# Kernel tuning notes

Hardware: AMD Instinct MI355X
Metric: run time of the kernel (lower is better)

Reference implementation:

```python
import jax, jax.numpy as jnp
import numpy as np

N_ATOMS = 200_000
N_EDGES = 10_000_000
N_MOL = 128


def setup_inputs() -> dict:
    key = jax.random.key(0)
    k1, k2, k3, k4, k5, k6, k7 = jax.random.split(key, 7)
    dEdRij = jax.random.normal(k1, (N_EDGES, 3), dtype=jnp.float32)
    Rij = jax.random.normal(k2, (N_EDGES, 3), dtype=jnp.float32)
    R = jax.random.normal(k3, (N_ATOMS, 3), dtype=jnp.float32)
    # Non-degenerate cells: ~10 Angstrom cubic boxes with small perturbation
    cell = jnp.eye(3, dtype=jnp.float32) * 10.0 + 0.1 * jax.random.normal(k4, (N_MOL, 3, 3), dtype=jnp.float32)
    idx_i = jax.random.randint(k5, (N_EDGES,), 0, N_ATOMS, dtype=jnp.int32)
    idx_j = jax.random.randint(k6, (N_EDGES,), 0, N_ATOMS, dtype=jnp.int32)
    idx_m = jnp.sort(jax.random.randint(k7, (N_ATOMS,), 0, N_MOL, dtype=jnp.int32))
    return {"dEdRij": dEdRij, "Rij": Rij, "R": R, "cell": cell,
            "idx_i": idx_i, "idx_j": idx_j, "idx_m": idx_m}


def reference(dEdRij, Rij, R, cell, idx_i, idx_j, idx_m):
    N = R.shape[0]
    M = cell.shape[0]
    # Forces: F = sum_{edges into i} dE/dRij - sum_{edges from j} dE/dRij
    forces = jnp.zeros_like(R).at[idx_i].add(dEdRij).at[idx_j].add(-dEdRij)
    # Per-edge outer product [E,3,3]: Rij[:, :, None] * dEdRij[:, None, :]
    stress_edge = dEdRij[:, None, :] * Rij[:, :, None]
    # Scatter to atoms, then reduce atoms -> molecules
    stress_i = jnp.zeros((N, 3, 3), dtype=R.dtype).at[idx_i].add(stress_edge)
    stress = jax.ops.segment_sum(stress_i, idx_m, num_segments=M)  # [M,3,3]
    # Cell volume via scalar triple product a . (b x c)
    volume = jnp.sum(cell[:, 0, :] * jnp.cross(cell[:, 1, :], cell[:, 2, :]), axis=1)  # [M]
    stress_out = (stress / volume[:, None, None]).reshape(M * 3, 3)
    return forces, stress_out
```

## Files before the change

### kernel.cpp

```cpp
#include <hip/hip_runtime.h>
#include <hip/hip_bf16.h>
#include <hip/hip_fp16.h>

#define N_MOL 128
#define STRESS_FLOATS (N_MOL * 9)
#define NB 128
#define APB 1563
#define NPAD (NB * APB)
#define EPB 1024
#define K_PT 4
#define BLK 256
#define RS_SLICES 64

__global__ void zero_f32_kernel(float* __restrict__ p, size_t n) {
    size_t i = (size_t)blockIdx.x * blockDim.x + threadIdx.x;
    if (i < n) p[i] = 0.f;
}

__device__ __forceinline__ unsigned short h16(float v) {
    return __half_as_ushort(__float2half_rn(v));
}

__global__ void __launch_bounds__(256)
scatter_kernel(const float* __restrict__ dEdRij,
               const float* __restrict__ Rij,
               const int*   __restrict__ idx_i,
               const int*   __restrict__ idx_j,
               const int*   __restrict__ idx_m,
               uint2* __restrict__ rec,
               int*   __restrict__ cnt,
               float* __restrict__ spart,
               int e0_chunk, int n_edges_chunk, int CAP)
{
    __shared__ int           hist[NB];
    __shared__ int           excl[NB];
    __shared__ int           cur[NB];
    __shared__ int           shiftb[NB];
    __shared__ float         smem[STRESS_FLOATS];
    __shared__ uint2         stg[EPB * 2];
    __shared__ unsigned char stgb[EPB * 2];

    for (int t = threadIdx.x; t < NB; t += blockDim.x) hist[t] = 0;
    for (int t = threadIdx.x; t < STRESS_FLOATS; t += blockDim.x) smem[t] = 0.f;
    __syncthreads();

    const int be0 = e0_chunk + blockIdx.x * EPB;
    const int be1 = min(be0 + EPB, e0_chunk + n_edges_chunk);

    int ei[K_PT], ej[K_PT];
    #pragma unroll
    for (int k = 0; k < K_PT; ++k) {
        const int e = be0 + k * BLK + threadIdx.x;
        ei[k] = -1; ej[k] = -1;
        if (e < be1) {
            ei[k] = idx_i[e];
            ej[k] = idx_j[e];
            atomicAdd(&hist[ei[k] / APB], 1);
            atomicAdd(&hist[ej[k] / APB], 1);
        }
    }
    __syncthreads();

    if (threadIdx.x < 64) {
        const int l = threadIdx.x;
        const int a = hist[2 * l], b = hist[2 * l + 1];
        int s = a + b;
        #pragma unroll
        for (int off = 1; off < 64; off <<= 1) {
            const int v = __shfl_up(s, off, 64);
            if (l >= off) s += v;
        }
        const int excl_pair = s - (a + b);
        excl[2 * l]     = excl_pair;
        excl[2 * l + 1] = excl_pair + a;
    }
    __syncthreads();

    for (int t = threadIdx.x; t < NB; t += blockDim.x) {
        const int h  = hist[t];
        const int ex = excl[t];
        const int g  = h ? atomicAdd(&cnt[t], h) : 0;
        cur[t]    = ex;
        shiftb[t] = t * CAP + g - ex;
    }
    __syncthreads();

    #pragma unroll
    for (int k = 0; k < K_PT; ++k) {
        const int e = be0 + k * BLK + threadIdx.x;
        if (e >= be1) continue;
        const int i = ei[k], j = ej[k];
        const float dx = dEdRij[3*e+0], dy = dEdRij[3*e+1], dz = dEdRij[3*e+2];
        const float rx = Rij[3*e+0],    ry = Rij[3*e+1],    rz = Rij[3*e+2];

        const int m = idx_m[i];
        float* s = &smem[m * 9];
        atomicAdd(&s[0], rx * dx);
        atomicAdd(&s[1], rx * dy);
        atomicAdd(&s[2], rx * dz);
        atomicAdd(&s[3], ry * dx);
        atomicAdd(&s[4], ry * dy);
        atomicAdd(&s[5], ry * dz);
        atomicAdd(&s[6], rz * dx);
        atomicAdd(&s[7], rz * dy);
        atomicAdd(&s[8], rz * dz);

        const int bi = i / APB;
        const int li = i - bi * APB;
        uint2 q;
        q.x = ((unsigned)li << 16) | h16(dx);
        q.y = (unsigned)h16(dy) | ((unsigned)h16(dz) << 16);
        int p = atomicAdd(&cur[bi], 1);
        stg[p] = q; stgb[p] = (unsigned char)bi;

        const int bj = j / APB;
        const int lj = j - bj * APB;
        q.x = ((unsigned)lj << 16) | h16(-dx);
        q.y = (unsigned)h16(-dy) | ((unsigned)h16(-dz) << 16);
        p = atomicAdd(&cur[bj], 1);
        stg[p] = q; stgb[p] = (unsigned char)bj;
    }
    __syncthreads();

    const int total = 2 * (be1 - be0);
    for (int t = threadIdx.x; t < total; t += blockDim.x) {
        const int b = stgb[t];
        const int gidx = t + shiftb[b];
        if (gidx < (b + 1) * CAP)
            rec[gidx] = stg[t];
    }

    __syncthreads();
    float* sp = spart + (size_t)blockIdx.x * STRESS_FLOATS;
    for (int t = threadIdx.x; t < STRESS_FLOATS; t += blockDim.x)
        sp[t] += smem[t];
}

__global__ void __launch_bounds__(256)
accum_kernel(const uint2* __restrict__ rec,
             const int*   __restrict__ cnt,
             float* __restrict__ partial,
             int CAP, int S, int store)
{
    __shared__ float facc[APB * 3];
    const int b = blockIdx.x / S;
    const int s = blockIdx.x - b * S;
    for (int t = threadIdx.x; t < APB * 3; t += blockDim.x) facc[t] = 0.f;
    __syncthreads();

    int n = cnt[b];
    if (n > CAP) n = CAP;
    int r0 = (int)((long long)n * s / S);
    int r1 = (int)((long long)n * (s + 1) / S);
    const uint2* rb = rec + (size_t)b * CAP;

#define ACC1(w0, w1)                                                  \
    {                                                                 \
        const int   l  = (int)((w0) >> 16);                           \
        const float fx = __half2float(__ushort_as_half(               \
                             (unsigned short)((w0) & 0xffffu)));      \
        const float fy = __half2float(__ushort_as_half(               \
                             (unsigned short)((w1) & 0xffffu)));      \
        const float fz = __half2float(__ushort_as_half(               \
                             (unsigned short)((w1) >> 16)));          \
        atomicAdd(&facc[l * 3 + 0], fx);                              \
        atomicAdd(&facc[l * 3 + 1], fy);                              \
        atomicAdd(&facc[l * 3 + 2], fz);                              \
    }

    if (r0 < r1 && (r0 & 1)) {
        if (threadIdx.x == 0) { const uint2 q = rb[r0]; ACC1(q.x, q.y); }
        ++r0;
    }
    if (r0 < r1 && (r1 & 1)) {
        --r1;
        if (threadIdx.x == 0) { const uint2 q = rb[r1]; ACC1(q.x, q.y); }
    }
    const int npair = (r1 - r0) >> 1;
    const uint4* rp = (const uint4*)(rb + r0);

    int p = threadIdx.x;
    for (; p + 7 * BLK < npair; p += 8 * BLK) {
        uint4 q0 = rp[p];
        uint4 q1 = rp[p + 1 * BLK];
        uint4 q2 = rp[p + 2 * BLK];
        uint4 q3 = rp[p + 3 * BLK];
        uint4 q4 = rp[p + 4 * BLK];
        uint4 q5 = rp[p + 5 * BLK];
        uint4 q6 = rp[p + 6 * BLK];
        uint4 q7 = rp[p + 7 * BLK];
        ACC1(q0.x, q0.y); ACC1(q0.z, q0.w);
        ACC1(q1.x, q1.y); ACC1(q1.z, q1.w);
        ACC1(q2.x, q2.y); ACC1(q2.z, q2.w);
        ACC1(q3.x, q3.y); ACC1(q3.z, q3.w);
        ACC1(q4.x, q4.y); ACC1(q4.z, q4.w);
        ACC1(q5.x, q5.y); ACC1(q5.z, q5.w);
        ACC1(q6.x, q6.y); ACC1(q6.z, q6.w);
        ACC1(q7.x, q7.y); ACC1(q7.z, q7.w);
    }
    for (; p < npair; p += BLK) {
        const uint4 q = rp[p];
        ACC1(q.x, q.y); ACC1(q.z, q.w);
    }
#undef ACC1

    __syncthreads();
    float* pp = partial + ((size_t)s * NPAD + (size_t)b * APB) * 3;
    if (store) {
        for (int t = threadIdx.x; t < APB * 3; t += blockDim.x)
            pp[t] = facc[t];
    } else {
        for (int t = threadIdx.x; t < APB * 3; t += blockDim.x)
            pp[t] += facc[t];
    }
}

__global__ void final_forces_kernel(const float* __restrict__ partial,
                                    float* __restrict__ forces, int n3, int S)
{
    const int t = blockIdx.x * blockDim.x + threadIdx.x;
    if (t >= n3) return;
    float a = 0.f;
    for (int s = 0; s < S; ++s)
        a += partial[(size_t)s * NPAD * 3 + t];
    forces[t] = a;
}

__global__ void reduce_stress_stage1(const float* __restrict__ spart,
                                     float* __restrict__ stmp, int rows)
{
    const int t = blockIdx.x * blockDim.x + threadIdx.x;
    if (t >= STRESS_FLOATS * RS_SLICES) return;
    const int col = t % STRESS_FLOATS;
    const int sl  = t / STRESS_FLOATS;
    float acc = 0.f;
    for (int r = sl; r < rows; r += RS_SLICES)
        acc += spart[(size_t)r * STRESS_FLOATS + col];
    stmp[sl * STRESS_FLOATS + col] = acc;
}

__global__ void reduce_stress_stage2(const float* __restrict__ stmp,
                                     const float* __restrict__ cell,
                                     float* __restrict__ out_stress)
{
    const int t = blockIdx.x * blockDim.x + threadIdx.x;
    if (t >= STRESS_FLOATS) return;
    float acc = 0.f;
    for (int s = 0; s < RS_SLICES; ++s)
        acc += stmp[s * STRESS_FLOATS + t];
    const int m = t / 9;
    const float* c = &cell[m * 9];
    const float a0 = c[0], a1 = c[1], a2 = c[2];
    const float b0 = c[3], b1 = c[4], b2 = c[5];
    const float c0 = c[6], c1 = c[7], c2 = c[8];
    const float x0 = b1 * c2 - b2 * c1;
    const float x1 = b2 * c0 - b0 * c2;
    const float x2 = b0 * c1 - b1 * c0;
    const float vol = a0 * x0 + a1 * x1 + a2 * x2;
    out_stress[t] = acc / vol;
}

__global__ void zero_f64_kernel(double* __restrict__ p, int n) {
    int i = blockIdx.x * blockDim.x + threadIdx.x;
    if (i < n) p[i] = 0.0;
}

__global__ void __launch_bounds__(256)
edge_kernel_f64(const float* __restrict__ dEdRij,
                const float* __restrict__ Rij,
                const int*   __restrict__ idx_i,
                const int*   __restrict__ idx_j,
                const int*   __restrict__ idx_m,
                double* __restrict__ facc,
                float*  __restrict__ spart,
                int E)
{
    __shared__ float smem[STRESS_FLOATS];
    for (int t = threadIdx.x; t < STRESS_FLOATS; t += blockDim.x) smem[t] = 0.f;
    __syncthreads();
    const int stride = gridDim.x * blockDim.x;
    for (int e = blockIdx.x * blockDim.x + threadIdx.x; e < E; e += stride) {
        const int i = idx_i[e], j = idx_j[e];
        const float dx = dEdRij[3*e+0], dy = dEdRij[3*e+1], dz = dEdRij[3*e+2];
        const float rx = Rij[3*e+0],    ry = Rij[3*e+1],    rz = Rij[3*e+2];
        double* fi = facc + 3 * (size_t)i;
        unsafeAtomicAdd(fi + 0, (double) dx);
        unsafeAtomicAdd(fi + 1, (double) dy);
        unsafeAtomicAdd(fi + 2, (double) dz);
        double* fj = facc + 3 * (size_t)j;
        unsafeAtomicAdd(fj + 0, (double)-dx);
        unsafeAtomicAdd(fj + 1, (double)-dy);
        unsafeAtomicAdd(fj + 2, (double)-dz);
        const int m = idx_m[i];
        float* s = &smem[m * 9];
        atomicAdd(&s[0], rx*dx); atomicAdd(&s[1], rx*dy); atomicAdd(&s[2], rx*dz);
        atomicAdd(&s[3], ry*dx); atomicAdd(&s[4], ry*dy); atomicAdd(&s[5], ry*dz);
        atomicAdd(&s[6], rz*dx); atomicAdd(&s[7], rz*dy); atomicAdd(&s[8], rz*dz);
    }
    __syncthreads();
    float* sp = spart + (size_t)blockIdx.x * STRESS_FLOATS;
    for (int t = threadIdx.x; t < STRESS_FLOATS; t += blockDim.x) sp[t] = smem[t];
}

__global__ void reduce_forces_f64_kernel(const double* __restrict__ facc,
                                         float* __restrict__ forces, int n3)
{
    int t = blockIdx.x * blockDim.x + threadIdx.x;
    if (t < n3) forces[t] = (float)facc[t];
}

extern "C" void kernel_launch(void* const* d_in, const int* in_sizes, int n_in,
                              void* d_out, int out_size, void* d_ws, size_t ws_size,
                              hipStream_t stream)
{
    const float* dEdRij = (const float*)d_in[0];
    const float* Rij    = (const float*)d_in[1];
    const float* R      = (const float*)d_in[2];  (void)R;
    const float* cell   = (const float*)d_in[3];
    const int*   idx_i  = (const int*)d_in[4];
    const int*   idx_j  = (const int*)d_in[5];
    const int*   idx_m  = (const int*)d_in[6];

    const int E  = in_sizes[0] / 3;
    const int N  = in_sizes[2] / 3;
    const int n3 = N * 3;

    float* out        = (float*)d_out;
    float* forces     = out;
    float* stress_out = out + (size_t)n3;

    int nchunks = 0, SEG = 0, CAP = 0, ROWS = 0;
    size_t rec_u2 = 0, spart_f = 0;
    {
        const int cand[14][2] = {
            {2,8},{2,4},{3,8},{3,4},{4,8},{4,4},{2,2},{5,4},
            {8,4},{8,2},{10,2},{16,2},{20,2},{40,1}};
        for (int ci = 0; ci < 14; ++ci) {
            const int nc = cand[ci][0];
            const int S  = cand[ci][1];
            const int CH = (E + nc - 1) / nc;
            const long long mean = 2LL * CH / NB;
            int cap = (int)(mean + mean / 16 + 64);
            cap = (cap + 1) & ~1;
            const int rows = (CH + EPB - 1) / EPB;
            const size_t need = (size_t)NB * cap * sizeof(uint2)
                              + (size_t)rows * STRESS_FLOATS * sizeof(float)
                              + (size_t)nc * NB * sizeof(int)
                              + (size_t)RS_SLICES * STRESS_FLOATS * sizeof(float)
                              + (size_t)S * NPAD * 3 * sizeof(float)
                              + 256;
            if (need <= ws_size) {
                nchunks = nc; SEG = S; CAP = cap; ROWS = rows;
                rec_u2  = (size_t)NB * cap;
                spart_f = (size_t)rows * STRESS_FLOATS;
                break;
            }
        }
    }

    if (nchunks > 0) {
        uint2* rec   = (uint2*)d_ws;
        float* spart = (float*)(rec + rec_u2);
        int*   cnt   = (int*)(spart + spart_f);
        float* stmp  = (float*)(cnt + (size_t)nchunks * NB);
        float* part  = stmp + (size_t)RS_SLICES * STRESS_FLOATS;

        const size_t zf = spart_f + (size_t)nchunks * NB;
        zero_f32_kernel<<<(int)((zf + BLK - 1) / BLK), BLK, 0, stream>>>(
            spart, zf);

        const int CH = (E + nchunks - 1) / nchunks;
        int chunk = 0;
        for (int s = 0; s < E; s += CH, ++chunk) {
            const int ce = min(CH, E - s);
            const int nb = (ce + EPB - 1) / EPB;

            scatter_kernel<<<nb, BLK, 0, stream>>>(
                dEdRij, Rij, idx_i, idx_j, idx_m,
                rec, cnt + (size_t)chunk * NB, spart, s, ce, CAP);

            accum_kernel<<<NB * SEG, BLK, 0, stream>>>(
                rec, cnt + (size_t)chunk * NB, part, CAP, SEG,
                chunk == 0 ? 1 : 0);
        }

        final_forces_kernel<<<(n3 + BLK - 1) / BLK, BLK, 0, stream>>>(
            part, forces, n3, SEG);
        reduce_stress_stage1<<<(STRESS_FLOATS * RS_SLICES + BLK - 1) / BLK,
                               BLK, 0, stream>>>(spart, stmp, ROWS);
        reduce_stress_stage2<<<(STRESS_FLOATS + BLK - 1) / BLK, BLK, 0, stream>>>(
            stmp, cell, stress_out);
    } else {
        double* facc   = (double*)d_ws;
        float*  spartf = (float*)(facc + n3);

        zero_f64_kernel<<<(n3 + BLK - 1) / BLK, BLK, 0, stream>>>(facc, n3);
        edge_kernel_f64<<<2048, BLK, 0, stream>>>(
            dEdRij, Rij, idx_i, idx_j, idx_m, facc, spartf, E);
        reduce_forces_f64_kernel<<<(n3 + BLK - 1) / BLK, BLK, 0, stream>>>(
            facc, forces, n3);
        reduce_stress_stage1<<<(STRESS_FLOATS * RS_SLICES + BLK - 1) / BLK,
                               BLK, 0, stream>>>(
            spartf, (float*)(spartf + (size_t)2048 * STRESS_FLOATS), 2048);
        reduce_stress_stage2<<<(STRESS_FLOATS + BLK - 1) / BLK, BLK, 0, stream>>>(
            (float*)(spartf + (size_t)2048 * STRESS_FLOATS), cell, stress_out);
    }
}
```

Baseline: 945.0 us.

## Overlap scatter and accumulate phases across chunks with double-buffered records

```diff
diff --git a/kernel.cpp b/kernel.cpp
--- a/kernel.cpp
+++ b/kernel.cpp
@@ -12,51 +12,52 @@
 #define BLK 256
 #define RS_SLICES 64
 
-__global__ void zero_f32_kernel(float* __restrict__ p, size_t n) {
-    size_t i = (size_t)blockIdx.x * blockDim.x + threadIdx.x;
-    if (i < n) p[i] = 0.f;
+#define SCAT_LDS (4*NB*4 + STRESS_FLOATS*4 + EPB*2*8 + EPB*2)
+#define ACC_LDS  (APB*3*4)
+
+__global__ void zero_i32_kernel(int* __restrict__ p, int n) {
+    int i = blockIdx.x * blockDim.x + threadIdx.x;
+    if (i < n) p[i] = 0;
 }
 
 __device__ __forceinline__ unsigned short h16(float v) {
     return __half_as_ushort(__float2half_rn(v));
 }
 
-__global__ void __launch_bounds__(256)
-scatter_kernel(const float* __restrict__ dEdRij,
-               const float* __restrict__ Rij,
-               const int*   __restrict__ idx_i,
-               const int*   __restrict__ idx_j,
-               const int*   __restrict__ idx_m,
-               uint2* __restrict__ rec,
-               int*   __restrict__ cnt,
-               float* __restrict__ spart,
-               int e0_chunk, int n_edges_chunk, int CAP)
-{
-    __shared__ int           hist[NB];
-    __shared__ int           excl[NB];
-    __shared__ int           cur[NB];
-    __shared__ int           shiftb[NB];
-    __shared__ float         smem[STRESS_FLOATS];
-    __shared__ uint2         stg[EPB * 2];
-    __shared__ unsigned char stgb[EPB * 2];
+__device__ __forceinline__ void scatter_body(
+    const float* __restrict__ dEdRij, const float* __restrict__ Rij,
+    const int* __restrict__ idx_i, const int* __restrict__ idx_j,
+    const int* __restrict__ idx_m,
+    uint2* __restrict__ rec, int* __restrict__ cnt, float* __restrict__ spart,
+    int e0_chunk, int n_edges_chunk, int CAP, int sstore,
+    char* lds, int sblk)
+{
+    int*   hist   = (int*)lds;
+    int*   excl   = hist + NB;
+    int*   cur    = excl + NB;
+    int*   shiftb = cur + NB;
+    float* smem   = (float*)(shiftb + NB);
+    uint2* stg    = (uint2*)(smem + STRESS_FLOATS);
+    unsigned char* stgb = (unsigned char*)(stg + EPB * 2);
 
     for (int t = threadIdx.x; t < NB; t += blockDim.x) hist[t] = 0;
     for (int t = threadIdx.x; t < STRESS_FLOATS; t += blockDim.x) smem[t] = 0.f;
     __syncthreads();
 
-    const int be0 = e0_chunk + blockIdx.x * EPB;
+    const int be0 = e0_chunk + sblk * EPB;
     const int be1 = min(be0 + EPB, e0_chunk + n_edges_chunk);
 
-    int ei[K_PT], ej[K_PT];
+    int ei[K_PT], ej[K_PT], em[K_PT];
     #pragma unroll
     for (int k = 0; k < K_PT; ++k) {
         const int e = be0 + k * BLK + threadIdx.x;
-        ei[k] = -1; ej[k] = -1;
+        ei[k] = -1; ej[k] = -1; em[k] = 0;
         if (e < be1) {
             ei[k] = idx_i[e];
             ej[k] = idx_j[e];
             atomicAdd(&hist[ei[k] / APB], 1);
             atomicAdd(&hist[ej[k] / APB], 1);
+            em[k] = idx_m[ei[k]];
         }
     }
     __syncthreads();
@@ -93,8 +94,7 @@
         const float dx = dEdRij[3*e+0], dy = dEdRij[3*e+1], dz = dEdRij[3*e+2];
         const float rx = Rij[3*e+0],    ry = Rij[3*e+1],    rz = Rij[3*e+2];
 
-        const int m = idx_m[i];
-        float* s = &smem[m * 9];
+        float* s = &smem[em[k] * 9];
         atomicAdd(&s[0], rx * dx);
         atomicAdd(&s[1], rx * dy);
         atomicAdd(&s[2], rx * dz);
@@ -131,20 +131,24 @@
     }
 
     __syncthreads();
-    float* sp = spart + (size_t)blockIdx.x * STRESS_FLOATS;
-    for (int t = threadIdx.x; t < STRESS_FLOATS; t += blockDim.x)
-        sp[t] += smem[t];
-}
-
-__global__ void __launch_bounds__(256)
-accum_kernel(const uint2* __restrict__ rec,
-             const int*   __restrict__ cnt,
-             float* __restrict__ partial,
-             int CAP, int S, int store)
-{
-    __shared__ float facc[APB * 3];
-    const int b = blockIdx.x / S;
-    const int s = blockIdx.x - b * S;
+    float* sp = spart + (size_t)sblk * STRESS_FLOATS;
+    if (sstore) {
+        for (int t = threadIdx.x; t < STRESS_FLOATS; t += blockDim.x)
+            sp[t] = smem[t];
+    } else {
+        for (int t = threadIdx.x; t < STRESS_FLOATS; t += blockDim.x)
+            sp[t] += smem[t];
+    }
+}
+
+__device__ __forceinline__ void accum_body(
+    const uint2* __restrict__ rec, const int* __restrict__ cnt,
+    float* __restrict__ partial, int CAP, int S, int store,
+    char* lds, int ablk)
+{
+    float* facc = (float*)lds;
+    const int b = ablk / S;
+    const int s = ablk - b * S;
     for (int t = threadIdx.x; t < APB * 3; t += blockDim.x) facc[t] = 0.f;
     __syncthreads();
 
@@ -215,6 +219,26 @@
     }
 }
 
+__global__ void __launch_bounds__(256)
+combo_kernel(const float* __restrict__ dEdRij, const float* __restrict__ Rij,
+             const int* __restrict__ idx_i, const int* __restrict__ idx_j,
+             const int* __restrict__ idx_m,
+             uint2* __restrict__ rec_s, int* __restrict__ cnt_s,
+             float* __restrict__ spart, int e0, int ce, int sstore,
+             const uint2* __restrict__ rec_a, const int* __restrict__ cnt_a,
+             float* __restrict__ partial, int astore,
+             int CAP, int SEG, int nb_scatter)
+{
+    __shared__ __align__(16) char lds[SCAT_LDS];
+    if ((int)blockIdx.x < nb_scatter) {
+        scatter_body(dEdRij, Rij, idx_i, idx_j, idx_m, rec_s, cnt_s, spart,
+                     e0, ce, CAP, sstore, lds, blockIdx.x);
+    } else {
+        accum_body(rec_a, cnt_a, partial, CAP, SEG, astore,
+                   lds, blockIdx.x - nb_scatter);
+    }
+}
+
 __global__ void final_forces_kernel(const float* __restrict__ partial,
                                     float* __restrict__ forces, int n3, int S)
 {
@@ -332,10 +356,9 @@
     int nchunks = 0, SEG = 0, CAP = 0, ROWS = 0;
     size_t rec_u2 = 0, spart_f = 0;
     {
-        const int cand[14][2] = {
-            {2,8},{2,4},{3,8},{3,4},{4,8},{4,4},{2,2},{5,4},
-            {8,4},{8,2},{10,2},{16,2},{20,2},{40,1}};
-        for (int ci = 0; ci < 14; ++ci) {
+        const int cand[8][2] = {
+            {4,8},{4,4},{6,8},{6,4},{8,8},{8,4},{12,4},{16,2}};
+        for (int ci = 0; ci < 8; ++ci) {
             const int nc = cand[ci][0];
             const int S  = cand[ci][1];
             const int CH = (E + nc - 1) / nc;
@@ -343,7 +366,7 @@
             int cap = (int)(mean + mean / 16 + 64);
             cap = (cap + 1) & ~1;
             const int rows = (CH + EPB - 1) / EPB;
-            const size_t need = (size_t)NB * cap * sizeof(uint2)
+            const size_t need = 2u * (size_t)NB * cap * sizeof(uint2)
                               + (size_t)rows * STRESS_FLOATS * sizeof(float)
                               + (size_t)nc * NB * sizeof(int)
                               + (size_t)RS_SLICES * STRESS_FLOATS * sizeof(float)
@@ -359,29 +382,37 @@
     }
 
     if (nchunks > 0) {
-        uint2* rec   = (uint2*)d_ws;
-        float* spart = (float*)(rec + rec_u2);
+        uint2* rec0  = (uint2*)d_ws;
+        uint2* rec1  = rec0 + rec_u2;
+        float* spart = (float*)(rec1 + rec_u2);
         int*   cnt   = (int*)(spart + spart_f);
         float* stmp  = (float*)(cnt + (size_t)nchunks * NB);
         float* part  = stmp + (size_t)RS_SLICES * STRESS_FLOATS;
 
-        const size_t zf = spart_f + (size_t)nchunks * NB;
-        zero_f32_kernel<<<(int)((zf + BLK - 1) / BLK), BLK, 0, stream>>>(
-            spart, zf);
+        zero_i32_kernel<<<(nchunks * NB + BLK - 1) / BLK, BLK, 0, stream>>>(
+            cnt, nchunks * NB);
 
         const int CH = (E + nchunks - 1) / nchunks;
-        int chunk = 0;
-        for (int s = 0; s < E; s += CH, ++chunk) {
-            const int ce = min(CH, E - s);
-            const int nb = (ce + EPB - 1) / EPB;
-
-            scatter_kernel<<<nb, BLK, 0, stream>>>(
+        const int na = NB * SEG;
+
+        for (int c = 0; c <= nchunks; ++c) {
+            const int  s_e0  = c * CH;
+            const int  s_ce  = (c < nchunks) ? min(CH, E - s_e0) : 0;
+            const int  nb    = (c < nchunks) ? (s_ce + EPB - 1) / EPB : 0;
+            const bool has_a = (c > 0);
+            const int  grid  = nb + (has_a ? na : 0);
+            if (grid == 0) continue;
+
+            uint2* rs = (c & 1) ? rec1 : rec0;
+            uint2* ra = (c & 1) ? rec0 : rec1;
+
+            combo_kernel<<<grid, BLK, 0, stream>>>(
                 dEdRij, Rij, idx_i, idx_j, idx_m,
-                rec, cnt + (size_t)chunk * NB, spart, s, ce, CAP);
-
-            accum_kernel<<<NB * SEG, BLK, 0, stream>>>(
-                rec, cnt + (size_t)chunk * NB, part, CAP, SEG,
-                chunk == 0 ? 1 : 0);
+                rs, cnt + (size_t)c * NB, spart, s_e0, s_ce,
+                (c == 0) ? 1 : 0,
+                ra, cnt + (size_t)(c - 1) * NB, part,
+                (c == 1) ? 1 : 0,
+                CAP, SEG, nb);
         }
 
         final_forces_kernel<<<(n3 + BLK - 1) / BLK, BLK, 0, stream>>>(
```

Result: slower. 988.5 us (+4.6%).
